# Kernel optimization log

Measured on AMD Instinct MI355X. Metric: run time of the kernel, lower is better.

Reference implementation:

```python
import jax, jax.numpy as jnp
import numpy as np

N = 200000
C = 128
B = 4
HF, WF = 32, 88
IMG_H, IMG_W = 256, 704
STRIDE = 8
MAX_BEV_RANGE = 54.0
HID = max(C // 2, 32)
LN_EPS = 1e-5


def setup_inputs() -> dict:
    key = jax.random.key(0)
    ks = jax.random.split(key, 16)
    x = jax.random.normal(ks[0], (N, C), jnp.float32)
    bid = jax.random.randint(ks[1], (N, 1), 0, B)
    zi = jax.random.randint(ks[2], (N, 1), 0, 5)
    yi = jax.random.randint(ks[3], (N, 1), 0, 180)
    xi = jax.random.randint(ks[4], (N, 1), 0, 180)
    indices = jnp.concatenate([bid, zi, yi, xi], axis=1).astype(jnp.int32)
    voxel_size = jnp.array([0.075, 0.075, 0.2], jnp.float32)
    pc_range = jnp.array([-54.0, -54.0, -5.0, 54.0, 54.0, 3.0], jnp.float32)
    aug = jnp.tile(jnp.eye(4, dtype=jnp.float32)[None], (B, 1, 1)) + 0.01 * jax.random.normal(ks[5], (B, 4, 4), jnp.float32)
    # realistic pinhole lidar->image projection (depth = lidar +x)
    trans_base = np.array([[352.0, -560.0, 0.0, 0.0],
                           [128.0, 0.0, -560.0, 0.0],
                           [1.0, 0.0, 0.0, 0.0]], np.float32)
    trans = jnp.asarray(trans_base)[None] + 0.01 * jax.random.normal(ks[6], (B, 3, 4), jnp.float32)
    img_feats = jax.random.normal(ks[7], (B, C, HF, WF), jnp.float32)
    s = 0.05
    return {
        'x': x, 'indices': indices, 'voxel_size': voxel_size, 'pc_range': pc_range,
        'lidar_aug_matrix': aug, 'trans_lidar_to_img': trans, 'img_feats': img_feats,
        'W1_fg': s * jax.random.normal(ks[8], (C, HID), jnp.float32),
        'b1_fg': jnp.zeros((HID,), jnp.float32),
        'W2_fg': s * jax.random.normal(ks[9], (HID, 1), jnp.float32),
        'b2_fg': jnp.zeros((1,), jnp.float32),
        'We1': s * jax.random.normal(ks[10], (2 * C, C), jnp.float32),
        'be1': jnp.zeros((C,), jnp.float32),
        'We2': s * jax.random.normal(ks[11], (C, C), jnp.float32),
        'be2': jnp.zeros((C,), jnp.float32),
        'ln_gamma': jnp.ones((C,), jnp.float32),
        'ln_beta': jnp.zeros((C,), jnp.float32),
        'img_h': IMG_H, 'img_w': IMG_W,
    }


def _bilinear_gather(img_feats, batch_ids, u_norm, v_norm):
    # F.grid_sample(align_corners=True, padding_mode='zeros'), batched via per-point gather
    _, _, H, W = img_feats.shape
    xp = (u_norm + 1.0) * 0.5 * (W - 1)
    yp = (v_norm + 1.0) * 0.5 * (H - 1)
    x0 = jnp.floor(xp)
    y0 = jnp.floor(yp)
    wx1 = xp - x0
    wy1 = yp - y0

    def corner(xi, yi):
        ok = (xi >= 0) & (xi <= W - 1) & (yi >= 0) & (yi <= H - 1)
        xc = jnp.clip(xi, 0, W - 1).astype(jnp.int32)
        yc = jnp.clip(yi, 0, H - 1).astype(jnp.int32)
        return img_feats[batch_ids, :, yc, xc] * ok[:, None]  # [N, C]

    f00 = corner(x0, y0)
    f01 = corner(x0 + 1, y0)
    f10 = corner(x0, y0 + 1)
    f11 = corner(x0 + 1, y0 + 1)
    w00 = ((1 - wx1) * (1 - wy1))[:, None]
    w01 = (wx1 * (1 - wy1))[:, None]
    w10 = ((1 - wx1) * wy1)[:, None]
    w11 = (wx1 * wy1)[:, None]
    return w00 * f00 + w01 * f01 + w10 * f10 + w11 * f11


def reference(x, indices, voxel_size, pc_range, lidar_aug_matrix, trans_lidar_to_img, img_feats,
              W1_fg, b1_fg, W2_fg, b2_fg, We1, be1, We2, be2, ln_gamma, ln_beta, img_h, img_w):
    bids = indices[:, 0].astype(jnp.int32)
    # voxel centers: indices cols (z,y,x) -> (x,y,z)
    spatial = indices[:, jnp.array([3, 2, 1])].astype(jnp.float32)
    cvs = voxel_size * STRIDE
    centers = spatial * cvs + pc_range[:3] + cvs * 0.5  # [N, 3]
    range_norm = jnp.linalg.norm(centers[:, :2], axis=-1, keepdims=True)
    range_norm = jnp.clip(range_norm / max(MAX_BEV_RANGE, 1e-6), 0.0, 1.0)

    xyz_hom = jnp.concatenate([centers, jnp.ones((centers.shape[0], 1), centers.dtype)], axis=1)
    aug_inv = jnp.linalg.inv(lidar_aug_matrix)[bids]  # [N, 4, 4]
    xyz_hom = jnp.einsum('nij,nj->ni', aug_inv, xyz_hom)
    pts = jnp.einsum('nij,nj->ni', trans_lidar_to_img[bids], xyz_hom)  # [N, 3]
    depth = pts[:, 2]
    safe_depth = jnp.maximum(depth, 1e-5)
    u_img = pts[:, 0] / safe_depth
    v_img = pts[:, 1] / safe_depth
    Hf, Wf = img_feats.shape[2], img_feats.shape[3]
    u_norm = 2.0 * (u_img * (float(Wf) / float(img_w))) / max(Wf - 1, 1) - 1.0
    v_norm = 2.0 * (v_img * (float(Hf) / float(img_h))) / max(Hf - 1, 1) - 1.0
    valid = (depth > 1e-5) & (jnp.abs(u_norm) <= 1.0) & (jnp.abs(v_norm) <= 1.0)  # [N]
    valid_f = valid.astype(x.dtype)[:, None]

    sampled_img = _bilinear_gather(img_feats, bids, u_norm, v_norm)  # [N, C]

    # ForegroundHead
    p_fg = jax.nn.sigmoid(jax.nn.relu(x @ W1_fg + b1_fg) @ W2_fg + b2_fg)
    # ConventionalFusionExpert with projection-valid mask
    h = jax.nn.relu(jnp.concatenate([x, sampled_img], axis=-1) @ We1 + be1)
    delta = (h @ We2 + be2) * valid_f

    gain = jnp.linalg.norm(delta, axis=-1, keepdims=True) / (jnp.linalg.norm(x, axis=-1, keepdims=True) + 1e-6)
    fusion_gain = jnp.clip(1.0 - jnp.exp(-gain), 0.0, 1.0)

    xr = x + delta
    mu = jnp.mean(xr, axis=-1, keepdims=True)
    var = jnp.mean(jnp.square(xr - mu), axis=-1, keepdims=True)
    x_out = (xr - mu) * jax.lax.rsqrt(var + LN_EPS) * ln_gamma + ln_beta

    return (x_out, p_fg, fusion_gain, range_norm, valid_f)
```

## Files before the change

### kernel.cpp

```cpp
#include <hip/hip_runtime.h>
#include <math.h>

#define CD  128
#define HFD 32
#define WFD 88

typedef __attribute__((ext_vector_type(4))) float  f4;
typedef __attribute__((ext_vector_type(8))) __bf16 b8;

__device__ __forceinline__ f4 mfma16(b8 a, b8 b, f4 c) {
  return __builtin_amdgcn_mfma_f32_16x16x32_bf16(a, b, c, 0, 0, 0);
}

__global__ void prep_inv_kernel(const float* __restrict__ aug,
                                float* __restrict__ auginv, int B) {
  int b = threadIdx.x;
  if (b >= B) return;
  double m[4][8];
  for (int i = 0; i < 4; ++i)
    for (int j = 0; j < 4; ++j) {
      m[i][j]     = (double)aug[b * 16 + i * 4 + j];
      m[i][4 + j] = (i == j) ? 1.0 : 0.0;
    }
  for (int col = 0; col < 4; ++col) {
    int piv = col;
    double best = fabs(m[col][col]);
    for (int r = col + 1; r < 4; ++r) {
      double v = fabs(m[r][col]);
      if (v > best) { best = v; piv = r; }
    }
    if (piv != col)
      for (int j = 0; j < 8; ++j) {
        double t = m[col][j]; m[col][j] = m[piv][j]; m[piv][j] = t;
      }
    double f = 1.0 / m[col][col];
    for (int j = 0; j < 8; ++j) m[col][j] *= f;
    for (int r = 0; r < 4; ++r)
      if (r != col) {
        double gg = m[r][col];
        for (int j = 0; j < 8; ++j) m[r][j] -= gg * m[col][j];
      }
  }
  for (int i = 0; i < 4; ++i)
    for (int j = 0; j < 4; ++j)
      auginv[b * 16 + i * 4 + j] = (float)m[i][4 + j];
}

__global__ void transpose_img_kernel(const float* __restrict__ img,
                                     __bf16* __restrict__ imgT, int total) {
  int o = blockIdx.x * blockDim.x + threadIdx.x;
  if (o >= total) return;
  int c   = o & (CD - 1);
  int pos = o >> 7;
  int xw  = pos % WFD;
  int tmp = pos / WFD;
  int yh  = tmp & (HFD - 1);
  int b   = tmp >> 5;
  imgT[o] = (__bf16)img[((b * CD + c) * HFD + yh) * WFD + xw];
}

__global__ void pack_weights_kernel(const float* __restrict__ W1,
                                    const float* __restrict__ We1,
                                    const float* __restrict__ We2,
                                    short* __restrict__ W1t,
                                    short* __restrict__ We1t,
                                    short* __restrict__ We2t) {
  int i = blockIdx.x * 256 + threadIdx.x;
  const float* W; short* O; int KB, Nw, idx; bool cmap;
  if (i < 8192)       { W = W1;  O = W1t;  KB = 4; Nw = 64;  idx = i;         cmap = true;  }
  else if (i < 40960) { W = We1; O = We1t; KB = 8; Nw = 128; idx = i - 8192;  cmap = true;  }
  else if (i < 57344) { W = We2; O = We2t; KB = 4; Nw = 128; idx = i - 40960; cmap = false; }
  else return;
  const int j    = idx & 7;
  const int lane = (idx >> 3) & 63;
  const int blk  = idx >> 9;
  const int kb   = blk % KB, mb = blk / KB;
  const int ch   = 16 * mb + (lane & 15);
  const int k    = cmap ? (32 * kb + 8 * (lane >> 4) + j)
                        : (32 * kb + 4 * (lane >> 4) + (j & 3) + 16 * (j >> 2));
  __bf16 h = (__bf16)W[k * Nw + ch];
  short s;
  __builtin_memcpy(&s, &h, 2);
  O[idx] = s;
}

__device__ __forceinline__ void geo_cat(
    int nc, int g, const float* __restrict__ x,
    const int* __restrict__ indices, const __bf16* __restrict__ imgT,
    const float* __restrict__ auginv, const float* __restrict__ trans,
    float vsx, float vsy, float vsz, float pcx, float pcy, float pcz,
    float su, float sv, b8* catf, float& vf_o, float& rn_o) {
  const int4 idx = *reinterpret_cast<const int4*>(indices + (size_t)nc * 4);
  const int  b   = idx.x;
  const float cx = (float)idx.w * vsx + pcx + 0.5f * vsx;
  const float cy = (float)idx.z * vsy + pcy + 0.5f * vsy;
  const float cz = (float)idx.y * vsz + pcz + 0.5f * vsz;

  const f4 A0 = *reinterpret_cast<const f4*>(auginv + b * 16 + 0);
  const f4 A1 = *reinterpret_cast<const f4*>(auginv + b * 16 + 4);
  const f4 A2 = *reinterpret_cast<const f4*>(auginv + b * 16 + 8);
  const f4 A3 = *reinterpret_cast<const f4*>(auginv + b * 16 + 12);
  const float h0 = A0[0] * cx + A0[1] * cy + A0[2] * cz + A0[3];
  const float h1 = A1[0] * cx + A1[1] * cy + A1[2] * cz + A1[3];
  const float h2 = A2[0] * cx + A2[1] * cy + A2[2] * cz + A2[3];
  const float h3 = A3[0] * cx + A3[1] * cy + A3[2] * cz + A3[3];
  const f4 T0 = *reinterpret_cast<const f4*>(trans + b * 12 + 0);
  const f4 T1 = *reinterpret_cast<const f4*>(trans + b * 12 + 4);
  const f4 T2 = *reinterpret_cast<const f4*>(trans + b * 12 + 8);
  const float q0    = T0[0] * h0 + T0[1] * h1 + T0[2] * h2 + T0[3] * h3;
  const float q1    = T1[0] * h0 + T1[1] * h1 + T1[2] * h2 + T1[3] * h3;
  const float depth = T2[0] * h0 + T2[1] * h1 + T2[2] * h2 + T2[3] * h3;
  const float safe  = fmaxf(depth, 1e-5f);
  const float u = q0 / safe, v = q1 / safe;
  const float un = 2.0f * (u * su) / 87.0f - 1.0f;
  const float vn = 2.0f * (v * sv) / 31.0f - 1.0f;
  vf_o = (depth > 1e-5f && fabsf(un) <= 1.0f && fabsf(vn) <= 1.0f) ? 1.0f : 0.0f;
  float rn = sqrtf(cx * cx + cy * cy) / 54.0f;
  rn_o = fminf(fmaxf(rn, 0.0f), 1.0f);

  const float xp  = (un + 1.0f) * 0.5f * 87.0f;
  const float yp  = (vn + 1.0f) * 0.5f * 31.0f;
  const float x0f = floorf(xp), y0f = floorf(yp);
  const float wx1 = xp - x0f, wy1 = yp - y0f;
  const float wx0 = 1.0f - wx1, wy0 = 1.0f - wy1;
  const bool okx0 = (x0f >= 0.0f) && (x0f <= 87.0f);
  const bool okx1 = (x0f + 1.0f >= 0.0f) && (x0f + 1.0f <= 87.0f);
  const bool oky0 = (y0f >= 0.0f) && (y0f <= 31.0f);
  const bool oky1 = (y0f + 1.0f >= 0.0f) && (y0f + 1.0f <= 31.0f);
  const int ix0 = (int)fminf(fmaxf(x0f, 0.0f), 87.0f);
  const int ix1 = (int)fminf(fmaxf(x0f + 1.0f, 0.0f), 87.0f);
  const int iy0 = (int)fminf(fmaxf(y0f, 0.0f), 31.0f);
  const int iy1 = (int)fminf(fmaxf(y0f + 1.0f, 0.0f), 31.0f);
  const float w00 = (okx0 && oky0) ? (wx0 * wy0) : 0.0f;
  const float w01 = (okx1 && oky0) ? (wx1 * wy0) : 0.0f;
  const float w10 = (okx0 && oky1) ? (wx0 * wy1) : 0.0f;
  const float w11 = (okx1 && oky1) ? (wx1 * wy1) : 0.0f;
  const int o00 = (iy0 * WFD + ix0) * CD;
  const int o01 = (iy0 * WFD + ix1) * CD;
  const int o10 = (iy1 * WFD + ix0) * CD;
  const int o11 = (iy1 * WFD + ix1) * CD;
  const __bf16* ib = imgT + (size_t)b * (HFD * WFD * CD);

  const float* xr = x + (size_t)nc * CD + 8 * g;
#pragma unroll
  for (int kb = 0; kb < 4; ++kb) {
    const f4 a = *reinterpret_cast<const f4*>(xr + 32 * kb);
    const f4 c = *reinterpret_cast<const f4*>(xr + 32 * kb + 4);
    b8 t;
#pragma unroll
    for (int e = 0; e < 4; ++e) {
      t[e]     = (__bf16)a[e];
      t[4 + e] = (__bf16)c[e];
    }
    catf[kb] = t;
  }
#pragma unroll
  for (int kb = 0; kb < 4; ++kb) {
    const int off = 32 * kb + 8 * g;
    const b8 f00 = *reinterpret_cast<const b8*>(ib + o00 + off);
    const b8 f01 = *reinterpret_cast<const b8*>(ib + o01 + off);
    const b8 f10 = *reinterpret_cast<const b8*>(ib + o10 + off);
    const b8 f11 = *reinterpret_cast<const b8*>(ib + o11 + off);
    b8 t;
#pragma unroll
    for (int e = 0; e < 8; ++e) {
      const float s = w00 * (float)f00[e] + w01 * (float)f01[e] +
                      w10 * (float)f10[e] + w11 * (float)f11[e];
      t[e] = (__bf16)s;
    }
    catf[4 + kb] = t;
  }
}

__device__ __forceinline__ void epilogue_pt(
    const f4* acc3, float vf, float rn, float sfg, int n, int nc, int g, int N,
    const float* __restrict__ x, const float* __restrict__ lng,
    const float* __restrict__ lnb, const float* __restrict__ b2,
    float* __restrict__ out, size_t OFF_PFG, size_t OFF_GAIN, size_t OFF_RN,
    size_t OFF_VAL) {
  f4 xrv[8];
  float sd = 0.0f, sx2 = 0.0f, sr = 0.0f, sr2 = 0.0f;
#pragma unroll
  for (int mb = 0; mb < 8; ++mb) {
    const f4 xv = *reinterpret_cast<const f4*>(x + (size_t)nc * CD + 16 * mb + 4 * g);
    const f4 d  = acc3[mb] * vf;
    const f4 r  = xv + d;
    xrv[mb] = r;
#pragma unroll
    for (int e = 0; e < 4; ++e) {
      sd  += d[e] * d[e];
      sx2 += xv[e] * xv[e];
      sr  += r[e];
      sr2 += r[e] * r[e];
    }
  }
  sd  += __shfl_xor(sd, 16);  sd  += __shfl_xor(sd, 32);
  sx2 += __shfl_xor(sx2, 16); sx2 += __shfl_xor(sx2, 32);
  sr  += __shfl_xor(sr, 16);  sr  += __shfl_xor(sr, 32);
  sr2 += __shfl_xor(sr2, 16); sr2 += __shfl_xor(sr2, 32);

  const float mu   = sr * (1.0f / 128.0f);
  const float var  = sr2 * (1.0f / 128.0f) - mu * mu;
  const float rstd = rsqrtf(var + 1e-5f);
  const float gn   = sqrtf(sd) / (sqrtf(sx2) + 1e-6f);
  const float fgain = fminf(fmaxf(1.0f - expf(-gn), 0.0f), 1.0f);

  if (n < N) {
#pragma unroll
    for (int mb = 0; mb < 8; ++mb) {
      const f4 gm = *reinterpret_cast<const f4*>(lng + 16 * mb + 4 * g);
      const f4 bt = *reinterpret_cast<const f4*>(lnb + 16 * mb + 4 * g);
      const f4 o  = (xrv[mb] - mu) * rstd * gm + bt;
      *reinterpret_cast<f4*>(out + (size_t)n * CD + 16 * mb + 4 * g) = o;
    }
    if (g == 0) {
      out[OFF_PFG  + n] = 1.0f / (1.0f + expf(-(sfg + b2[0])));
      out[OFF_GAIN + n] = fgain;
      out[OFF_RN   + n] = rn;
      out[OFF_VAL  + n] = vf;
    }
  }
}

__global__ __launch_bounds__(768)
void fused_mfma_kernel(const float* __restrict__ x,
                       const int* __restrict__ indices,
                       const float* __restrict__ voxel_size,
                       const float* __restrict__ pc_range,
                       const float* __restrict__ trans,
                       const float* __restrict__ auginv,
                       const __bf16* __restrict__ imgT,
                       const short* __restrict__ wsrc,
                       const float* __restrict__ b1,
                       const float* __restrict__ W2,
                       const float* __restrict__ b2,
                       const float* __restrict__ be1,
                       const float* __restrict__ be2,
                       const float* __restrict__ lng,
                       const float* __restrict__ lnb,
                       const int* __restrict__ img_h_p,
                       const int* __restrict__ img_w_p,
                       float* __restrict__ out, int N) {
  __shared__ __align__(16) short wlds[57344];
  const int tid  = threadIdx.x;
  const int lane = tid & 63;
  const int wv   = tid >> 6;
  const int g    = lane >> 4;
  const int pl   = lane & 15;
  const int n0   = blockIdx.x * 384 + wv * 32 + pl;
  const int n1   = n0 + 16;
  const int nc0  = (n0 < N) ? n0 : (N - 1);
  const int nc1  = (n1 < N) ? n1 : (N - 1);

  const size_t NN       = (size_t)N;
  const size_t OFF_PFG  = NN * CD;
  const size_t OFF_GAIN = OFF_PFG + NN;
  const size_t OFF_RN   = OFF_GAIN + NN;
  const size_t OFF_VAL  = OFF_RN + NN;

#pragma unroll
  for (int i = 0; i < 10; ++i) {
    const int f = wv + i * 12;
    if (f < 112) {
      __builtin_amdgcn_global_load_lds(
          (const __attribute__((address_space(1))) unsigned int*)
              (wsrc + (size_t)f * 512 + lane * 8),
          (__attribute__((address_space(3))) unsigned int*)(wlds + f * 512),
          16, 0, 0);
    }
  }

  const float vsx = voxel_size[0] * 8.0f;
  const float vsy = voxel_size[1] * 8.0f;
  const float vsz = voxel_size[2] * 8.0f;
  const float pcx = pc_range[0], pcy = pc_range[1], pcz = pc_range[2];
  const float su  = (float)WFD / (float)(*img_w_p);
  const float sv  = (float)HFD / (float)(*img_h_p);

  b8 cat0[8], cat1[8];
  float vf0, rn0, vf1, rn1;
  geo_cat(nc0, g, x, indices, imgT, auginv, trans, vsx, vsy, vsz,
          pcx, pcy, pcz, su, sv, cat0, vf0, rn0);
  geo_cat(nc1, g, x, indices, imgT, auginv, trans, vsx, vsy, vsz,
          pcx, pcy, pcz, su, sv, cat1, vf1, rn1);

  __syncthreads();

  const short* wb = wlds + lane * 8;

  float sfg0 = 0.0f, sfg1 = 0.0f;
#pragma unroll
  for (int mb = 0; mb < 4; ++mb) {
    const f4 bi = *reinterpret_cast<const f4*>(b1 + 16 * mb + 4 * g);
    f4 a0 = bi, a1 = bi;
#pragma unroll
    for (int kb = 0; kb < 4; ++kb) {
      const b8 w = *reinterpret_cast<const b8*>(wb + (mb * 4 + kb) * 512);
      a0 = mfma16(w, cat0[kb], a0);
      a1 = mfma16(w, cat1[kb], a1);
    }
    const f4 w2v = *reinterpret_cast<const f4*>(W2 + 16 * mb + 4 * g);
#pragma unroll
    for (int e = 0; e < 4; ++e) {
      sfg0 += fmaxf(a0[e], 0.0f) * w2v[e];
      sfg1 += fmaxf(a1[e], 0.0f) * w2v[e];
    }
  }
  sfg0 += __shfl_xor(sfg0, 16); sfg0 += __shfl_xor(sfg0, 32);
  sfg1 += __shfl_xor(sfg1, 16); sfg1 += __shfl_xor(sfg1, 32);

  b8 b30[4], b31[4];
#pragma unroll
  for (int pr = 0; pr < 4; ++pr) {
    const f4 biA = *reinterpret_cast<const f4*>(be1 + 16 * (2 * pr) + 4 * g);
    const f4 biB = *reinterpret_cast<const f4*>(be1 + 16 * (2 * pr + 1) + 4 * g);
    f4 aA0 = biA, aB0 = biB, aA1 = biA, aB1 = biB;
#pragma unroll
    for (int kb = 0; kb < 8; ++kb) {
      const b8 wA = *reinterpret_cast<const b8*>(wb + (16 + (2 * pr) * 8 + kb) * 512);
      const b8 wB = *reinterpret_cast<const b8*>(wb + (16 + (2 * pr + 1) * 8 + kb) * 512);
      aA0 = mfma16(wA, cat0[kb], aA0);
      aB0 = mfma16(wB, cat0[kb], aB0);
      aA1 = mfma16(wA, cat1[kb], aA1);
      aB1 = mfma16(wB, cat1[kb], aB1);
    }
    b8 t0, t1;
#pragma unroll
    for (int e = 0; e < 4; ++e) {
      t0[e]     = (__bf16)fmaxf(aA0[e], 0.0f);
      t0[4 + e] = (__bf16)fmaxf(aB0[e], 0.0f);
      t1[e]     = (__bf16)fmaxf(aA1[e], 0.0f);
      t1[4 + e] = (__bf16)fmaxf(aB1[e], 0.0f);
    }
    b30[pr] = t0;
    b31[pr] = t1;
  }

  f4 acc30[8], acc31[8];
#pragma unroll
  for (int mb = 0; mb < 8; ++mb) {
    const f4 bi = *reinterpret_cast<const f4*>(be2 + 16 * mb + 4 * g);
    acc30[mb] = bi;
    acc31[mb] = bi;
  }
#pragma unroll
  for (int kb = 0; kb < 4; ++kb) {
#pragma unroll
    for (int mb = 0; mb < 8; ++mb) {
      const b8 w = *reinterpret_cast<const b8*>(wb + (80 + mb * 4 + kb) * 512);
      acc30[mb] = mfma16(w, b30[kb], acc30[mb]);
      acc31[mb] = mfma16(w, b31[kb], acc31[mb]);
    }
  }

  epilogue_pt(acc30, vf0, rn0, sfg0, n0, nc0, g, N, x, lng, lnb, b2, out,
              OFF_PFG, OFF_GAIN, OFF_RN, OFF_VAL);
  epilogue_pt(acc31, vf1, rn1, sfg1, n1, nc1, g, N, x, lng, lnb, b2, out,
              OFF_PFG, OFF_GAIN, OFF_RN, OFF_VAL);
}

extern "C" void kernel_launch(void* const* d_in, const int* in_sizes, int n_in,
                              void* d_out, int out_size, void* d_ws, size_t ws_size,
                              hipStream_t stream) {
  const float* x       = (const float*)d_in[0];
  const int*   indices = (const int*)d_in[1];
  const float* voxel   = (const float*)d_in[2];
  const float* pcr     = (const float*)d_in[3];
  const float* aug     = (const float*)d_in[4];
  const float* trans   = (const float*)d_in[5];
  const float* img     = (const float*)d_in[6];
  const float* W1      = (const float*)d_in[7];
  const float* b1      = (const float*)d_in[8];
  const float* W2      = (const float*)d_in[9];
  const float* b2      = (const float*)d_in[10];
  const float* We1     = (const float*)d_in[11];
  const float* be1     = (const float*)d_in[12];
  const float* We2     = (const float*)d_in[13];
  const float* be2     = (const float*)d_in[14];
  const float* lng     = (const float*)d_in[15];
  const float* lnb     = (const float*)d_in[16];
  const int*   img_h   = (const int*)d_in[17];
  const int*   img_w   = (const int*)d_in[18];

  const int N         = in_sizes[0] / CD;
  const int B         = in_sizes[4] / 16;
  const int img_total = in_sizes[6];
  const size_t IMG_BYTES = (size_t)img_total * 2;

  char*   wsb    = (char*)d_ws;
  float*  auginv = (float*)wsb;
  __bf16* imgT   = (__bf16*)(wsb + 1024);
  short*  W1t    = (short*)(wsb + 1024 + IMG_BYTES);
  short*  We1t   = W1t + 8192;
  short*  We2t   = We1t + 32768;

  prep_inv_kernel<<<1, 64, 0, stream>>>(aug, auginv, B);
  transpose_img_kernel<<<(img_total + 255) / 256, 256, 0, stream>>>(
      img, imgT, img_total);
  pack_weights_kernel<<<224, 256, 0, stream>>>(W1, We1, We2, W1t, We1t, We2t);
  fused_mfma_kernel<<<(N + 383) / 384, 768, 0, stream>>>(
      x, indices, voxel, pcr, trans, auginv, imgT,
      W1t, b1, W2, b2, be1, be2,
      lng, lnb, img_h, img_w, (float*)d_out, N);
}
```

Baseline: 139.0 us.

## Make fused MFMA kernel persistent so LDS weights load once per block

The fused kernel becomes a persistent grid of 256 blocks. Each wave loops over 32-point chunks in a grid stride, instead of launching one block per 384 points. The 112 KB weight tile is copied into LDS only once per block rather than once per 384 points, which cuts global and L2 weight traffic and the per-block startup cost. The trade-off is fewer resident blocks: 256 blocks of 768 threads on 256 CUs may leave occupancy low, and there is no explicit overlap of gather latency beyond what the compiler schedules.

```diff
diff --git a/kernel.cpp b/kernel.cpp
--- a/kernel.cpp
+++ b/kernel.cpp
@@ -240,17 +240,15 @@
                        const float* __restrict__ lnb,
                        const int* __restrict__ img_h_p,
                        const int* __restrict__ img_w_p,
-                       float* __restrict__ out, int N) {
+                       float* __restrict__ out, int N, int nchunks) {
   __shared__ __align__(16) short wlds[57344];
   const int tid  = threadIdx.x;
   const int lane = tid & 63;
   const int wv   = tid >> 6;
   const int g    = lane >> 4;
   const int pl   = lane & 15;
-  const int n0   = blockIdx.x * 384 + wv * 32 + pl;
-  const int n1   = n0 + 16;
-  const int nc0  = (n0 < N) ? n0 : (N - 1);
-  const int nc1  = (n1 < N) ? n1 : (N - 1);
+  const int wg   = blockIdx.x * 12 + wv;
+  const int NW   = gridDim.x * 12;
 
   const size_t NN       = (size_t)N;
   const size_t OFF_PFG  = NN * CD;
@@ -277,86 +275,106 @@
   const float su  = (float)WFD / (float)(*img_w_p);
   const float sv  = (float)HFD / (float)(*img_h_p);
 
+  int c = wg;
   b8 cat0[8], cat1[8];
   float vf0, rn0, vf1, rn1;
-  geo_cat(nc0, g, x, indices, imgT, auginv, trans, vsx, vsy, vsz,
-          pcx, pcy, pcz, su, sv, cat0, vf0, rn0);
-  geo_cat(nc1, g, x, indices, imgT, auginv, trans, vsx, vsy, vsz,
-          pcx, pcy, pcz, su, sv, cat1, vf1, rn1);
+  int n0 = 0, n1 = 0, nc0 = 0, nc1 = 0;
+  if (c < nchunks) {
+    n0 = c * 32 + pl;  n1 = n0 + 16;
+    nc0 = (n0 < N) ? n0 : (N - 1);
+    nc1 = (n1 < N) ? n1 : (N - 1);
+    geo_cat(nc0, g, x, indices, imgT, auginv, trans, vsx, vsy, vsz,
+            pcx, pcy, pcz, su, sv, cat0, vf0, rn0);
+    geo_cat(nc1, g, x, indices, imgT, auginv, trans, vsx, vsy, vsz,
+            pcx, pcy, pcz, su, sv, cat1, vf1, rn1);
+  }
 
   __syncthreads();
 
   const short* wb = wlds + lane * 8;
 
-  float sfg0 = 0.0f, sfg1 = 0.0f;
-#pragma unroll
-  for (int mb = 0; mb < 4; ++mb) {
-    const f4 bi = *reinterpret_cast<const f4*>(b1 + 16 * mb + 4 * g);
-    f4 a0 = bi, a1 = bi;
+  while (c < nchunks) {
+    float sfg0 = 0.0f, sfg1 = 0.0f;
+#pragma unroll
+    for (int mb = 0; mb < 4; ++mb) {
+      const f4 bi = *reinterpret_cast<const f4*>(b1 + 16 * mb + 4 * g);
+      f4 a0 = bi, a1 = bi;
+#pragma unroll
+      for (int kb = 0; kb < 4; ++kb) {
+        const b8 w = *reinterpret_cast<const b8*>(wb + (mb * 4 + kb) * 512);
+        a0 = mfma16(w, cat0[kb], a0);
+        a1 = mfma16(w, cat1[kb], a1);
+      }
+      const f4 w2v = *reinterpret_cast<const f4*>(W2 + 16 * mb + 4 * g);
+#pragma unroll
+      for (int e = 0; e < 4; ++e) {
+        sfg0 += fmaxf(a0[e], 0.0f) * w2v[e];
+        sfg1 += fmaxf(a1[e], 0.0f) * w2v[e];
+      }
+    }
+    sfg0 += __shfl_xor(sfg0, 16); sfg0 += __shfl_xor(sfg0, 32);
+    sfg1 += __shfl_xor(sfg1, 16); sfg1 += __shfl_xor(sfg1, 32);
+
+    b8 b30[4], b31[4];
+#pragma unroll
+    for (int pr = 0; pr < 4; ++pr) {
+      const f4 biA = *reinterpret_cast<const f4*>(be1 + 16 * (2 * pr) + 4 * g);
+      const f4 biB = *reinterpret_cast<const f4*>(be1 + 16 * (2 * pr + 1) + 4 * g);
+      f4 aA0 = biA, aB0 = biB, aA1 = biA, aB1 = biB;
+#pragma unroll
+      for (int kb = 0; kb < 8; ++kb) {
+        const b8 wA = *reinterpret_cast<const b8*>(wb + (16 + (2 * pr) * 8 + kb) * 512);
+        const b8 wB = *reinterpret_cast<const b8*>(wb + (16 + (2 * pr + 1) * 8 + kb) * 512);
+        aA0 = mfma16(wA, cat0[kb], aA0);
+        aB0 = mfma16(wB, cat0[kb], aB0);
+        aA1 = mfma16(wA, cat1[kb], aA1);
+        aB1 = mfma16(wB, cat1[kb], aB1);
+      }
+      b8 t0, t1;
+#pragma unroll
+      for (int e = 0; e < 4; ++e) {
+        t0[e]     = (__bf16)fmaxf(aA0[e], 0.0f);
+        t0[4 + e] = (__bf16)fmaxf(aB0[e], 0.0f);
+        t1[e]     = (__bf16)fmaxf(aA1[e], 0.0f);
+        t1[4 + e] = (__bf16)fmaxf(aB1[e], 0.0f);
+      }
+      b30[pr] = t0;
+      b31[pr] = t1;
+    }
+
+    f4 acc30[8], acc31[8];
+#pragma unroll
+    for (int mb = 0; mb < 8; ++mb) {
+      const f4 bi = *reinterpret_cast<const f4*>(be2 + 16 * mb + 4 * g);
+      acc30[mb] = bi;
+      acc31[mb] = bi;
+    }
 #pragma unroll
     for (int kb = 0; kb < 4; ++kb) {
-      const b8 w = *reinterpret_cast<const b8*>(wb + (mb * 4 + kb) * 512);
-      a0 = mfma16(w, cat0[kb], a0);
-      a1 = mfma16(w, cat1[kb], a1);
-    }
-    const f4 w2v = *reinterpret_cast<const f4*>(W2 + 16 * mb + 4 * g);
-#pragma unroll
-    for (int e = 0; e < 4; ++e) {
-      sfg0 += fmaxf(a0[e], 0.0f) * w2v[e];
-      sfg1 += fmaxf(a1[e], 0.0f) * w2v[e];
-    }
-  }
-  sfg0 += __shfl_xor(sfg0, 16); sfg0 += __shfl_xor(sfg0, 32);
-  sfg1 += __shfl_xor(sfg1, 16); sfg1 += __shfl_xor(sfg1, 32);
-
-  b8 b30[4], b31[4];
-#pragma unroll
-  for (int pr = 0; pr < 4; ++pr) {
-    const f4 biA = *reinterpret_cast<const f4*>(be1 + 16 * (2 * pr) + 4 * g);
-    const f4 biB = *reinterpret_cast<const f4*>(be1 + 16 * (2 * pr + 1) + 4 * g);
-    f4 aA0 = biA, aB0 = biB, aA1 = biA, aB1 = biB;
-#pragma unroll
-    for (int kb = 0; kb < 8; ++kb) {
-      const b8 wA = *reinterpret_cast<const b8*>(wb + (16 + (2 * pr) * 8 + kb) * 512);
-      const b8 wB = *reinterpret_cast<const b8*>(wb + (16 + (2 * pr + 1) * 8 + kb) * 512);
-      aA0 = mfma16(wA, cat0[kb], aA0);
-      aB0 = mfma16(wB, cat0[kb], aB0);
-      aA1 = mfma16(wA, cat1[kb], aA1);
-      aB1 = mfma16(wB, cat1[kb], aB1);
-    }
-    b8 t0, t1;
-#pragma unroll
-    for (int e = 0; e < 4; ++e) {
-      t0[e]     = (__bf16)fmaxf(aA0[e], 0.0f);
-      t0[4 + e] = (__bf16)fmaxf(aB0[e], 0.0f);
-      t1[e]     = (__bf16)fmaxf(aA1[e], 0.0f);
-      t1[4 + e] = (__bf16)fmaxf(aB1[e], 0.0f);
-    }
-    b30[pr] = t0;
-    b31[pr] = t1;
-  }
-
-  f4 acc30[8], acc31[8];
-#pragma unroll
-  for (int mb = 0; mb < 8; ++mb) {
-    const f4 bi = *reinterpret_cast<const f4*>(be2 + 16 * mb + 4 * g);
-    acc30[mb] = bi;
-    acc31[mb] = bi;
-  }
-#pragma unroll
-  for (int kb = 0; kb < 4; ++kb) {
-#pragma unroll
-    for (int mb = 0; mb < 8; ++mb) {
-      const b8 w = *reinterpret_cast<const b8*>(wb + (80 + mb * 4 + kb) * 512);
-      acc30[mb] = mfma16(w, b30[kb], acc30[mb]);
-      acc31[mb] = mfma16(w, b31[kb], acc31[mb]);
-    }
-  }
-
-  epilogue_pt(acc30, vf0, rn0, sfg0, n0, nc0, g, N, x, lng, lnb, b2, out,
-              OFF_PFG, OFF_GAIN, OFF_RN, OFF_VAL);
-  epilogue_pt(acc31, vf1, rn1, sfg1, n1, nc1, g, N, x, lng, lnb, b2, out,
-              OFF_PFG, OFF_GAIN, OFF_RN, OFF_VAL);
+#pragma unroll
+      for (int mb = 0; mb < 8; ++mb) {
+        const b8 w = *reinterpret_cast<const b8*>(wb + (80 + mb * 4 + kb) * 512);
+        acc30[mb] = mfma16(w, b30[kb], acc30[mb]);
+        acc31[mb] = mfma16(w, b31[kb], acc31[mb]);
+      }
+    }
+
+    epilogue_pt(acc30, vf0, rn0, sfg0, n0, nc0, g, N, x, lng, lnb, b2, out,
+                OFF_PFG, OFF_GAIN, OFF_RN, OFF_VAL);
+    epilogue_pt(acc31, vf1, rn1, sfg1, n1, nc1, g, N, x, lng, lnb, b2, out,
+                OFF_PFG, OFF_GAIN, OFF_RN, OFF_VAL);
+
+    c += NW;
+    if (c < nchunks) {
+      n0 = c * 32 + pl;  n1 = n0 + 16;
+      nc0 = (n0 < N) ? n0 : (N - 1);
+      nc1 = (n1 < N) ? n1 : (N - 1);
+      geo_cat(nc0, g, x, indices, imgT, auginv, trans, vsx, vsy, vsz,
+              pcx, pcy, pcz, su, sv, cat0, vf0, rn0);
+      geo_cat(nc1, g, x, indices, imgT, auginv, trans, vsx, vsy, vsz,
+              pcx, pcy, pcz, su, sv, cat1, vf1, rn1);
+    }
+  }
 }
 
 extern "C" void kernel_launch(void* const* d_in, const int* in_sizes, int n_in,
@@ -385,6 +403,7 @@
   const int N         = in_sizes[0] / CD;
   const int B         = in_sizes[4] / 16;
   const int img_total = in_sizes[6];
+  const int nchunks   = (N + 31) / 32;
   const size_t IMG_BYTES = (size_t)img_total * 2;
 
   char*   wsb    = (char*)d_ws;
@@ -398,8 +417,8 @@
   transpose_img_kernel<<<(img_total + 255) / 256, 256, 0, stream>>>(
       img, imgT, img_total);
   pack_weights_kernel<<<224, 256, 0, stream>>>(W1, We1, We2, W1t, We1t, We2t);
-  fused_mfma_kernel<<<(N + 383) / 384, 768, 0, stream>>>(
+  fused_mfma_kernel<<<256, 768, 0, stream>>>(
       x, indices, voxel, pcr, trans, auginv, imgT,
       W1t, b1, W2, b2, be1, be2,
-      lng, lnb, img_h, img_w, (float*)d_out, N);
-}
+      lng, lnb, img_h, img_w, (float*)d_out, N, nchunks);
+}
```

Result: slower. 475.5 us (+242.0%).
